# Kernel optimization log

Measured on AMD Instinct MI355X. Metric: run time of the kernel, lower is better.

The kernel has to match this reference:

```python
import jax, jax.numpy as jnp
import numpy as np

B = 8192
NV = 778   # MANO vertices
NJ = 16    # LBS joints
PARENTS = np.array([0, 0, 1, 2, 0, 4, 5, 0, 7, 8, 0, 10, 11, 0, 13, 14])


def quat2mat(quat):
    # quat: [N,4] (w,x,y,z) -> [N,3,3]
    q = quat / jnp.linalg.norm(quat, axis=1, keepdims=True)
    w, x, y, z = q[:, 0], q[:, 1], q[:, 2], q[:, 3]
    w2, x2, y2, z2 = w * w, x * x, y * y, z * z
    wx, wy, wz = w * x, w * y, w * z
    xy, xz, yz = x * y, x * z, y * z
    R = jnp.stack([
        w2 + x2 - y2 - z2, 2 * xy - 2 * wz, 2 * wy + 2 * xz,
        2 * wz + 2 * xy, w2 - x2 + y2 - z2, 2 * yz - 2 * wx,
        2 * xz - 2 * wy, 2 * wx + 2 * yz, w2 - x2 - y2 + z2,
    ], axis=1)
    return R.reshape(-1, 3, 3)


def batch_rodrigues(theta):
    # theta: [N,3] axis-angle -> [N,3,3]
    angle = jnp.linalg.norm(theta + 1e-8, axis=1, keepdims=True)
    normalized = theta / angle
    half = angle * 0.5
    quat = jnp.concatenate([jnp.cos(half), jnp.sin(half) * normalized], axis=1)
    return quat2mat(quat)


def qmul(q, r):
    # Hamilton product, (w,x,y,z); q,r: [N,4]
    w1, x1, y1, z1 = q[:, 0], q[:, 1], q[:, 2], q[:, 3]
    w2, x2, y2, z2 = r[:, 0], r[:, 1], r[:, 2], r[:, 3]
    return jnp.stack([
        w1 * w2 - x1 * x2 - y1 * y2 - z1 * z2,
        w1 * x2 + x1 * w2 + y1 * z2 - z1 * y2,
        w1 * y2 - x1 * z2 + y1 * w2 + z1 * x2,
        w1 * z2 + x1 * y2 - y1 * x2 + z1 * w2,
    ], axis=1)


def make_A(R, t):
    # R: [B,J,3,3], t: [B,J,3] -> [B,J,4,4]
    Bn, J = R.shape[0], R.shape[1]
    top = jnp.concatenate([R, t[..., None]], axis=-1)              # [B,J,3,4]
    bot = jnp.broadcast_to(jnp.array([0., 0., 0., 1.], R.dtype), (Bn, J, 1, 4))
    return jnp.concatenate([top, bot], axis=-2)


def mano_forward(theta, delta_quat, user_shape, init_quat, init_trans,
                 v_template, shapedirs, J_regressor, posedirs, weights):
    Bn = theta.shape[0]
    beta = jnp.broadcast_to(user_shape, (Bn, user_shape.shape[-1]))
    v_shaped = (beta @ shapedirs).reshape(Bn, NV, 3) + v_template   # [B,778,3]
    J = jnp.einsum('bvc,vj->bjc', v_shaped, J_regressor)            # [B,21,3]

    Rs = batch_rodrigues(theta.reshape(-1, 3)).reshape(Bn, 15, 3, 3)
    pose_feature = (Rs - jnp.eye(3, dtype=Rs.dtype)).reshape(Bn, 135)
    v_posed = (pose_feature @ posedirs).reshape(Bn, NV, 3) + v_shaped

    quat = qmul(delta_quat, jnp.broadcast_to(init_quat, (Bn, 4)))
    root_R = quat2mat(quat)                                          # [B,3,3]
    Rs_all = jnp.concatenate([root_R[:, None], Rs], axis=1)          # [B,16,3,3]

    Jk = J[:, :NJ]                                                   # [B,16,3]
    rel = Jk - Jk[:, PARENTS]
    rel = rel.at[:, 0].set(Jk[:, 0])                                 # root keeps absolute pos
    A_local = make_A(Rs_all, rel)                                    # [B,16,4,4]

    # kinematic chain (fixed 16-joint tree)
    results = [A_local[:, 0]]
    for i in range(1, NJ):
        results.append(results[PARENTS[i]] @ A_local[:, i])
    G = jnp.stack(results, axis=1)                                   # [B,16,4,4]

    Jw0 = jnp.concatenate([Jk, jnp.zeros((Bn, NJ, 1), Jk.dtype)], axis=-1)
    init_bone = jnp.einsum('bjkl,bjl->bjk', G, Jw0)                  # [B,16,4]
    A = jnp.concatenate([G[..., :3], G[..., 3:] - init_bone[..., None]], axis=-1)

    T = jnp.einsum('vj,bjkl->bvkl', weights, A)                      # [B,778,4,4]
    vp_homo = jnp.concatenate([v_posed, jnp.ones((Bn, NV, 1), v_posed.dtype)], axis=-1)
    verts = jnp.einsum('bvkl,bvl->bvk', T, vp_homo)[..., :3]         # [B,778,3]

    joints = jnp.einsum('bvc,vj->bjc', verts, J_regressor)           # [B,21,3]
    trans = init_trans.reshape(Bn, 1, 3)
    return joints + trans  # get_skin=False path


def setup_inputs() -> dict:
    key = jax.random.key(0)
    ks = jax.random.split(key, 10)
    return {
        'theta': jax.random.normal(ks[0], (B, 45), jnp.float32) * 0.3,
        'delta_quat': jax.random.normal(ks[1], (B, 4), jnp.float32),
        'user_shape': jax.random.normal(ks[2], (1, 10), jnp.float32),
        'init_quat': jax.random.normal(ks[3], (1, 4), jnp.float32),
        'init_trans': jax.random.normal(ks[4], (B, 3), jnp.float32),
        'v_template': jax.random.normal(ks[5], (NV, 3), jnp.float32),
        'shapedirs': jax.random.normal(ks[6], (10, NV * 3), jnp.float32) * 0.01,
        'J_regressor': jax.random.uniform(ks[7], (NV, 21), jnp.float32) / NV,
        'posedirs': jax.random.normal(ks[8], (135, NV * 3), jnp.float32) * 0.01,
        'weights': jax.random.uniform(ks[9], (NV, NJ), jnp.float32),
    }


def reference(theta, delta_quat, user_shape, init_quat, init_trans,
              v_template, shapedirs, J_regressor, posedirs, weights):
    return mano_forward(theta, delta_quat, user_shape, init_quat, init_trans,
                        v_template, shapedirs, J_regressor, posedirs, weights)
```

## Files before the change

### kernel.cpp

```cpp
#include <hip/hip_runtime.h>
#include <math.h>

#define B_SIZE 8192
#define NVERT 778
#define NP 135
#define NEC 416
#define KS16 16

#define OFF_JK    0
#define OFF_C1    64
#define OFF_C0    400
#define OFF_P2    1408
#define OFF_PFT   137488
#define OFF_AT    1243408
#define OFF_PP_OVER 137488
#define OFF_PP_SAFE 2816272

__device__ inline void quat2mat_dev(float qw, float qx, float qy, float qz, float* R) {
  float n = sqrtf(qw*qw + qx*qx + qy*qy + qz*qz);
  float w = qw/n, x = qx/n, y = qy/n, z = qz/n;
  float w2=w*w, x2=x*x, y2=y*y, z2=z*z;
  float wx=w*x, wy=w*y, wz=w*z, xy=x*y, xz=x*z, yz=y*z;
  R[0]=w2+x2-y2-z2; R[1]=2.f*xy-2.f*wz; R[2]=2.f*wy+2.f*xz;
  R[3]=2.f*wz+2.f*xy; R[4]=w2-x2+y2-z2; R[5]=2.f*yz-2.f*wx;
  R[6]=2.f*xz-2.f*wy; R[7]=2.f*wx+2.f*yz; R[8]=w2-x2-y2+z2;
}

__device__ inline void rodrigues_dev(float tx, float ty, float tz, float* R) {
  float ax = tx + 1e-8f, ay = ty + 1e-8f, az = tz + 1e-8f;
  float angle = sqrtf(ax*ax + ay*ay + az*az);
  float nx = tx/angle, ny = ty/angle, nz = tz/angle;
  float half = 0.5f*angle;
  float cw = cosf(half), sw = sinf(half);
  quat2mat_dev(cw, sw*nx, sw*ny, sw*nz, R);
}

__device__ inline void pose_unit(const float* __restrict__ theta,
                                 const float* __restrict__ delta_quat,
                                 const float* __restrict__ init_quat,
                                 float* __restrict__ ws,
                                 const float* jk, const float* rel,
                                 int bb, int u, int lane) {
  int b = bb*256 + lane;
  float* pfT = ws + OFF_PFT;
  float4* AT4 = (float4*)(ws + OFF_AT);
  float w1=delta_quat[b*4+0], x1=delta_quat[b*4+1], y1=delta_quat[b*4+2], z1=delta_quat[b*4+3];
  float w2=init_quat[0], x2=init_quat[1], y2=init_quat[2], z2=init_quat[3];
  float qw = w1*w2 - x1*x2 - y1*y2 - z1*z2;
  float qx = w1*x2 + x1*w2 + y1*z2 - z1*y2;
  float qy = w1*y2 - x1*z2 + y1*w2 + z1*x2;
  float qz = w1*z2 + x1*y2 - y1*x2 + z1*w2;
  float G[12];
  quat2mat_dev(qw, qx, qy, qz, G);
  G[9] = rel[0]; G[10] = rel[1]; G[11] = rel[2];
  if (u == 5) {
    #pragma unroll
    for (int c = 0; c < 3; ++c) {
      float g0 = G[c*3+0], g1 = G[c*3+1], g2 = G[c*3+2];
      AT4[(size_t)(c)*B_SIZE + b] =
        make_float4(g0, g1, g2, G[9+c] - (g0*jk[0] + g1*jk[1] + g2*jk[2]));
    }
    return;
  }
  #pragma unroll
  for (int mstep = 0; mstep < 3; ++mstep) {
    int j = 3*u + 1 + mstep;
    int i = j - 1;
    float R[9];
    rodrigues_dev(theta[b*45+3*i+0], theta[b*45+3*i+1], theta[b*45+3*i+2], R);
    pfT[(size_t)(9*i+0)*B_SIZE + b] = R[0]-1.f;
    pfT[(size_t)(9*i+1)*B_SIZE + b] = R[1];
    pfT[(size_t)(9*i+2)*B_SIZE + b] = R[2];
    pfT[(size_t)(9*i+3)*B_SIZE + b] = R[3];
    pfT[(size_t)(9*i+4)*B_SIZE + b] = R[4]-1.f;
    pfT[(size_t)(9*i+5)*B_SIZE + b] = R[5];
    pfT[(size_t)(9*i+6)*B_SIZE + b] = R[6];
    pfT[(size_t)(9*i+7)*B_SIZE + b] = R[7];
    pfT[(size_t)(9*i+8)*B_SIZE + b] = R[8]-1.f;
    float nG[12];
    const float* rj = rel + j*3;
    #pragma unroll
    for (int r3 = 0; r3 < 3; ++r3) {
      float a0 = G[r3*3+0], a1 = G[r3*3+1], a2 = G[r3*3+2];
      nG[r3*3+0] = a0*R[0] + a1*R[3] + a2*R[6];
      nG[r3*3+1] = a0*R[1] + a1*R[4] + a2*R[7];
      nG[r3*3+2] = a0*R[2] + a1*R[5] + a2*R[8];
      nG[9+r3]   = G[9+r3] + a0*rj[0] + a1*rj[1] + a2*rj[2];
    }
    #pragma unroll
    for (int k = 0; k < 12; ++k) G[k] = nG[k];
    const float* jkj = jk + j*3;
    #pragma unroll
    for (int c = 0; c < 3; ++c) {
      float g0 = G[c*3+0], g1 = G[c*3+1], g2 = G[c*3+2];
      AT4[(size_t)(j*3+c)*B_SIZE + b] =
        make_float4(g0, g1, g2, G[9+c] - (g0*jkj[0] + g1*jkj[1] + g2*jkj[2]));
    }
  }
}

__device__ inline void kr_task(float* __restrict__ ws, int pp_off, int idx) {
  if (idx >= 416*84) return;
  int ec = idx / 84, q4 = idx - ec*84;
  const float* Pp = ws + pp_off;
  float4 s = make_float4(0.f, 0.f, 0.f, 0.f);
  #pragma unroll
  for (int ks = 0; ks < KS16; ++ks) {
    float4 v = *(const float4*)&Pp[(size_t)ks*NEC*336 + ec*336 + 4*q4];
    s.x += v.x; s.y += v.y; s.z += v.z; s.w += v.w;
  }
  float sv[4] = {s.x, s.y, s.z, s.w};
  #pragma unroll
  for (int r = 0; r < 4; ++r) {
    int q2 = 4*q4 + r;
    int jj2 = q2 >> 4, jj = q2 & 15;
    if (ec < 408) {
      int c = ec / 136, pp = ec - c*136;
      if (pp < 135) ws[OFF_P2 + (size_t)(jj2*135 + pp)*48 + jj*3 + c] = sv[r];
      else          ws[OFF_C0 + jj2*48 + jj*3 + c] = sv[r];
    } else if (ec == 408) {
      ws[OFF_C1 + jj2*16 + jj] = sv[r];
    }
  }
}

__global__ __launch_bounds__(256) void kA(const float* __restrict__ J_regressor,
                                          const float* __restrict__ weights,
                                          const float* __restrict__ posedirs,
                                          const float* __restrict__ user_shape,
                                          const float* __restrict__ v_template,
                                          const float* __restrict__ shapedirs,
                                          float* __restrict__ ws, int pp_off) {
  int tid = threadIdx.x;
  int bid = blockIdx.x;

  if (bid >= 416) {
    int j = bid - 416;
    __shared__ float red[3*256];
    __shared__ float ush[10];
    if (tid < 10) ush[tid] = user_shape[tid];
    __syncthreads();
    float p0 = 0.f, p1 = 0.f, p2 = 0.f;
    for (int v = tid; v < NVERT; v += 256) {
      float jr = J_regressor[v*21 + j];
      #pragma unroll
      for (int c = 0; c < 3; ++c) {
        int e = 3*v + c;
        float t = v_template[e];
        #pragma unroll
        for (int s = 0; s < 10; ++s) t += ush[s]*shapedirs[s*2334 + e];
        float val = jr * t;
        if (c == 0) p0 += val; else if (c == 1) p1 += val; else p2 += val;
      }
    }
    red[0*256+tid] = p0; red[1*256+tid] = p1; red[2*256+tid] = p2;
    __syncthreads();
    for (int s = 128; s > 0; s >>= 1) {
      if (tid < s) {
        red[0*256+tid] += red[0*256+tid+s];
        red[1*256+tid] += red[1*256+tid+s];
        red[2*256+tid] += red[2*256+tid+s];
      }
      __syncthreads();
    }
    if (tid < 3) ws[OFF_JK + j*3 + tid] = red[tid*256];
    return;
  }

  __shared__ float sJR[49*21];
  __shared__ float sW [49*16];
  __shared__ float sB [64*16];
  __shared__ float ush[10];
  if (tid < 10) ush[tid] = user_shape[tid];
  int ng = bid % 26;
  int ks = bid / 26;
  int vbeg = ks*49;
  int kt = min(NVERT - vbeg, 49);
  __syncthreads();
  for (int idx = tid; idx < kt*21; idx += 256) sJR[idx] = J_regressor[vbeg*21 + idx];
  for (int idx = tid; idx < kt*16; idx += 256) sW[idx]  = weights[vbeg*16 + idx];
  for (int idx = tid; idx < 16*64; idx += 256) {
    int s = idx >> 6, iv = idx & 63;
    if (iv < kt) {
      int ec = ng*16 + s;
      float val;
      if (ec > 408) val = 0.f;
      else if (ec == 408) val = 1.f;
      else {
        int c = ec / 136, pp = ec - c*136;
        int e = 3*(vbeg+iv) + c;
        if (pp == 135) {
          float t = v_template[e];
          #pragma unroll
          for (int s0 = 0; s0 < 10; ++s0) t += ush[s0]*shapedirs[s0*2334 + e];
          val = t;
        } else {
          val = posedirs[pp*2334 + e];
        }
      }
      sB[iv*16 + s] = val;
    }
  }
  __syncthreads();
  if (tid < 168) {
    int cg2 = (tid < 84) ? 0 : 1;
    int r4  = (tid < 84) ? tid : tid - 84;
    int q2 = 4*r4;
    int j2 = q2 >> 4;
    int jb = q2 & 15;
    float acc[4][8];
    #pragma unroll
    for (int r = 0; r < 4; ++r)
      #pragma unroll
      for (int s = 0; s < 8; ++s) acc[r][s] = 0.f;
    for (int i = 0; i < kt; ++i) {
      float jr = sJR[i*21 + j2];
      float4 w4 = *(const float4*)&sW[i*16 + jb];
      float4 b0 = *(const float4*)&sB[i*16 + cg2*8];
      float4 b1 = *(const float4*)&sB[i*16 + cg2*8 + 4];
      float wv[4] = {w4.x, w4.y, w4.z, w4.w};
      #pragma unroll
      for (int r = 0; r < 4; ++r) {
        float s2 = jr * wv[r];
        acc[r][0] += s2*b0.x; acc[r][1] += s2*b0.y;
        acc[r][2] += s2*b0.z; acc[r][3] += s2*b0.w;
        acc[r][4] += s2*b1.x; acc[r][5] += s2*b1.y;
        acc[r][6] += s2*b1.z; acc[r][7] += s2*b1.w;
      }
    }
    float* Pp = ws + pp_off + (size_t)ks*NEC*336;
    #pragma unroll
    for (int s = 0; s < 8; ++s) {
      int ec = ng*16 + cg2*8 + s;
      float4 v4 = make_float4(acc[0][s], acc[1][s], acc[2][s], acc[3][s]);
      *(float4*)&Pp[ec*336 + q2] = v4;
    }
  }
}

__global__ __launch_bounds__(256) void kRk4(const float* __restrict__ theta,
                                            const float* __restrict__ delta_quat,
                                            const float* __restrict__ init_quat,
                                            float* __restrict__ ws, int pp_off) {
  int bid = blockIdx.x;
  int tid = threadIdx.x;
  if (bid < 137) {
    kr_task(ws, pp_off, bid*256 + tid);
    return;
  }
  __shared__ float jk[48], rel[48];
  if (tid < 48) {
    float v = ws[OFF_JK + tid];
    jk[tid] = v;
    int j = tid/3, c = tid - j*3;
    float r;
    if (j == 0) r = v;
    else {
      int par = (((j-1) % 3) == 0) ? 0 : (j-1);
      r = v - ws[OFF_JK + par*3 + c];
    }
    rel[tid] = r;
  }
  __syncthreads();
  int s = bid & 7;
  int t = (bid - 137) >> 3;
  int bb = s + 8*(t & 3);
  int u  = t >> 2;
  pose_unit(theta, delta_quat, init_quat, ws, jk, rel, bb, u, tid);
}

__global__ void kR_fb(float* __restrict__ ws, int pp_off) {
  kr_task(ws, pp_off, blockIdx.x*256 + threadIdx.x);
}

__global__ __launch_bounds__(256) void k4_fb(const float* __restrict__ theta,
                                             const float* __restrict__ delta_quat,
                                             const float* __restrict__ init_quat,
                                             float* __restrict__ ws) {
  int bid = blockIdx.x;
  int tid = threadIdx.x;
  __shared__ float jk[48], rel[48];
  if (tid < 48) {
    float v = ws[OFF_JK + tid];
    jk[tid] = v;
    int j = tid/3, c = tid - j*3;
    float r;
    if (j == 0) r = v;
    else {
      int par = (((j-1) % 3) == 0) ? 0 : (j-1);
      r = v - ws[OFF_JK + par*3 + c];
    }
    rel[tid] = r;
  }
  __syncthreads();
  int s = bid & 7;
  int t = bid >> 3;
  int bb = s + 8*(t & 3);
  int u  = t >> 2;
  pose_unit(theta, delta_quat, init_quat, ws, jk, rel, bb, u, tid);
}

__global__ __launch_bounds__(256) void k5_main(const float* __restrict__ init_trans,
                                               const float* __restrict__ ws,
                                               float* __restrict__ out) {
  __shared__ __align__(16) float4 sP2[NP*12];
  int g = blockIdx.x;
  int xcd = g & 7, k = g >> 3;
  int br  = ((k & 3) << 3) | xcd;
  int j2  = k >> 2;
  int tid = threadIdx.x;
  int b   = br*256 + tid;

  const float4* P2g = (const float4*)(ws + OFF_P2) + j2*NP*12;
  for (int i = tid; i < NP*12; i += 256) sP2[i] = P2g[i];
  __syncthreads();

  float4 acc[12];
  const float4* c04 = (const float4*)(ws + OFF_C0 + j2*48);
  #pragma unroll
  for (int i = 0; i < 12; ++i) acc[i] = c04[i];

  const float* pfT = ws + OFF_PFT;
  #pragma unroll 3
  for (int p = 0; p < NP; ++p) {
    float pf = pfT[(size_t)p*B_SIZE + b];
    const float4* Pr = &sP2[p*12];
    #pragma unroll
    for (int i = 0; i < 12; ++i) {
      float4 pv = Pr[i];
      acc[i].x += pf*pv.x; acc[i].y += pf*pv.y;
      acc[i].z += pf*pv.z; acc[i].w += pf*pv.w;
    }
  }

  float m[48];
  #pragma unroll
  for (int i = 0; i < 12; ++i) {
    m[4*i+0] = acc[i].x; m[4*i+1] = acc[i].y;
    m[4*i+2] = acc[i].z; m[4*i+3] = acc[i].w;
  }

  const float4* AT4 = (const float4*)(ws + OFF_AT);
  const float* c1p = ws + OFF_C1 + j2*16;
  float o0 = 0.f, o1 = 0.f, o2 = 0.f;
  #pragma unroll
  for (int j = 0; j < 16; ++j) {
    float c1 = c1p[j];
    float m0 = m[3*j+0], m1 = m[3*j+1], m2 = m[3*j+2];
    #pragma unroll
    for (int k2 = 0; k2 < 3; ++k2) {
      float4 a = AT4[(size_t)(j*3+k2)*B_SIZE + b];
      float r = a.x*m0 + a.y*m1 + a.z*m2 + a.w*c1;
      if (k2 == 0) o0 += r; else if (k2 == 1) o1 += r; else o2 += r;
    }
  }
  size_t ob = ((size_t)b*21 + j2)*3;
  out[ob+0] = o0 + init_trans[b*3+0];
  out[ob+1] = o1 + init_trans[b*3+1];
  out[ob+2] = o2 + init_trans[b*3+2];
}

extern "C" void kernel_launch(void* const* d_in, const int* in_sizes, int n_in,
                              void* d_out, int out_size, void* d_ws, size_t ws_size,
                              hipStream_t stream) {
  const float* theta       = (const float*)d_in[0];
  const float* delta_quat  = (const float*)d_in[1];
  const float* user_shape  = (const float*)d_in[2];
  const float* init_quat   = (const float*)d_in[3];
  const float* init_trans  = (const float*)d_in[4];
  const float* v_template  = (const float*)d_in[5];
  const float* shapedirs   = (const float*)d_in[6];
  const float* J_regressor = (const float*)d_in[7];
  const float* posedirs    = (const float*)d_in[8];
  const float* weights     = (const float*)d_in[9];
  float* out = (float*)d_out;
  float* ws  = (float*)d_ws;

  size_t need = ((size_t)OFF_PP_SAFE + (size_t)KS16*NEC*336) * 4;
  if (ws_size >= need) {
    kA<<<432, 256, 0, stream>>>(J_regressor, weights, posedirs,
                                user_shape, v_template, shapedirs, ws, OFF_PP_SAFE);
    kRk4<<<329, 256, 0, stream>>>(theta, delta_quat, init_quat, ws, OFF_PP_SAFE);
  } else {
    kA<<<432, 256, 0, stream>>>(J_regressor, weights, posedirs,
                                user_shape, v_template, shapedirs, ws, OFF_PP_OVER);
    kR_fb<<<137, 256, 0, stream>>>(ws, OFF_PP_OVER);
    k4_fb<<<192, 256, 0, stream>>>(theta, delta_quat, init_quat, ws);
  }
  k5_main<<<672, 256, 0, stream>>>(init_trans, ws, out);
}
```

Measured before the change: 167.7 us.

## Compute two batch rows per thread in k5 and read P2 from global via uniform offset

The final kernel now runs 128 threads per block, and each thread handles two batch elements (b and b+128) instead of one. The shared-memory staging of the P2 coefficient table is removed. P2 is instead read straight from global memory through a block-uniform offset, so the loads can become scalar/constant-cache reads shared by both accumulators. This removes the LDS fill and barrier cost and reuses each P2 value for two rows, at the price of doubled accumulator registers (96 float accumulators) and possibly lower occupancy or spills.

```diff
diff --git a/kernel.cpp b/kernel.cpp
--- a/kernel.cpp
+++ b/kernel.cpp
@@ -300,64 +300,81 @@
   pose_unit(theta, delta_quat, init_quat, ws, jk, rel, bb, u, tid);
 }
 
-__global__ __launch_bounds__(256) void k5_main(const float* __restrict__ init_trans,
+__global__ __launch_bounds__(128) void k5_main(const float* __restrict__ init_trans,
                                                const float* __restrict__ ws,
                                                float* __restrict__ out) {
-  __shared__ __align__(16) float4 sP2[NP*12];
+  __shared__ int s_voff[1];
   int g = blockIdx.x;
   int xcd = g & 7, k = g >> 3;
   int br  = ((k & 3) << 3) | xcd;
   int j2  = k >> 2;
   int tid = threadIdx.x;
   int b   = br*256 + tid;
-
-  const float4* P2g = (const float4*)(ws + OFF_P2) + j2*NP*12;
-  for (int i = tid; i < NP*12; i += 256) sP2[i] = P2g[i];
+  int b2  = b + 128;
+
+  if (tid == 0) s_voff[0] = j2*135*12;
   __syncthreads();
-
-  float4 acc[12];
+  int voff = s_voff[0];
+
+  float4 acc[12], acc2[12];
   const float4* c04 = (const float4*)(ws + OFF_C0 + j2*48);
   #pragma unroll
-  for (int i = 0; i < 12; ++i) acc[i] = c04[i];
+  for (int i = 0; i < 12; ++i) { acc[i] = c04[i]; acc2[i] = acc[i]; }
 
   const float* pfT = ws + OFF_PFT;
+  const float4* P24 = (const float4*)(ws + OFF_P2) + voff;
   #pragma unroll 3
   for (int p = 0; p < NP; ++p) {
-    float pf = pfT[(size_t)p*B_SIZE + b];
-    const float4* Pr = &sP2[p*12];
+    float pf  = pfT[(size_t)p*B_SIZE + b];
+    float pf2 = pfT[(size_t)p*B_SIZE + b2];
+    const float4* Pr = P24 + p*12;
     #pragma unroll
     for (int i = 0; i < 12; ++i) {
       float4 pv = Pr[i];
-      acc[i].x += pf*pv.x; acc[i].y += pf*pv.y;
-      acc[i].z += pf*pv.z; acc[i].w += pf*pv.w;
-    }
-  }
-
-  float m[48];
+      acc[i].x  += pf *pv.x; acc[i].y  += pf *pv.y;
+      acc[i].z  += pf *pv.z; acc[i].w  += pf *pv.w;
+      acc2[i].x += pf2*pv.x; acc2[i].y += pf2*pv.y;
+      acc2[i].z += pf2*pv.z; acc2[i].w += pf2*pv.w;
+    }
+  }
+
+  float m[48], m2[48];
   #pragma unroll
   for (int i = 0; i < 12; ++i) {
-    m[4*i+0] = acc[i].x; m[4*i+1] = acc[i].y;
-    m[4*i+2] = acc[i].z; m[4*i+3] = acc[i].w;
+    m[4*i+0]  = acc[i].x;  m[4*i+1]  = acc[i].y;
+    m[4*i+2]  = acc[i].z;  m[4*i+3]  = acc[i].w;
+    m2[4*i+0] = acc2[i].x; m2[4*i+1] = acc2[i].y;
+    m2[4*i+2] = acc2[i].z; m2[4*i+3] = acc2[i].w;
   }
 
   const float4* AT4 = (const float4*)(ws + OFF_AT);
   const float* c1p = ws + OFF_C1 + j2*16;
   float o0 = 0.f, o1 = 0.f, o2 = 0.f;
+  float q0 = 0.f, q1 = 0.f, q2v = 0.f;
   #pragma unroll
   for (int j = 0; j < 16; ++j) {
     float c1 = c1p[j];
-    float m0 = m[3*j+0], m1 = m[3*j+1], m2 = m[3*j+2];
+    float m0  = m[3*j+0],  m1  = m[3*j+1],  mm2 = m[3*j+2];
+    float n0  = m2[3*j+0], n1  = m2[3*j+1], n2  = m2[3*j+2];
     #pragma unroll
     for (int k2 = 0; k2 < 3; ++k2) {
-      float4 a = AT4[(size_t)(j*3+k2)*B_SIZE + b];
-      float r = a.x*m0 + a.y*m1 + a.z*m2 + a.w*c1;
-      if (k2 == 0) o0 += r; else if (k2 == 1) o1 += r; else o2 += r;
+      float4 a  = AT4[(size_t)(j*3+k2)*B_SIZE + b];
+      float4 a2 = AT4[(size_t)(j*3+k2)*B_SIZE + b2];
+      float r  = a.x *m0 + a.y *m1 + a.z *mm2 + a.w *c1;
+      float r2 = a2.x*n0 + a2.y*n1 + a2.z*n2  + a2.w*c1;
+      if (k2 == 0) { o0 += r; q0 += r2; }
+      else if (k2 == 1) { o1 += r; q1 += r2; }
+      else { o2 += r; q2v += r2; }
     }
   }
   size_t ob = ((size_t)b*21 + j2)*3;
   out[ob+0] = o0 + init_trans[b*3+0];
   out[ob+1] = o1 + init_trans[b*3+1];
   out[ob+2] = o2 + init_trans[b*3+2];
+  size_t ob2 = ((size_t)b2*21 + j2)*3;
+  out[ob2+0] = q0  + init_trans[b2*3+0];
+  out[ob2+1] = q1  + init_trans[b2*3+1];
+  out[ob2+2] = q2v + init_trans[b2*3+2];
 }
 
 extern "C" void kernel_launch(void* const* d_in, const int* in_sizes, int n_in,
@@ -387,5 +404,5 @@
     kR_fb<<<137, 256, 0, stream>>>(ws, OFF_PP_OVER);
     k4_fb<<<192, 256, 0, stream>>>(theta, delta_quat, init_quat, ws);
   }
-  k5_main<<<672, 256, 0, stream>>>(init_trans, ws, out);
-}
+  k5_main<<<672, 128, 0, stream>>>(init_trans, ws, out);
+}
```

After: 158.1 us. 5.8% less time.
